# Kernel optimization log

Hardware: AMD Instinct MI355X
Metric: run time of the kernel (lower is better)

Reference implementation:

```python
import jax, jax.numpy as jnp
import numpy as np

N_EMBD = 512
N_HEAD = 8


def setup_inputs() -> dict:
    key = jax.random.key(0)
    k_x, k_aw, k_ab, k_pw, k_pb = jax.random.split(key, 5)
    B, T, E = 4, 2048, N_EMBD
    s = 1.0 / np.sqrt(E)
    return {
        "x": jax.random.normal(k_x, (B, T, E), dtype=jnp.float32),
        # torch Linear weight is [out, in]; store transposed for x @ W
        "c_attn_w": jax.random.uniform(k_aw, (E, 3 * E), jnp.float32, -s, s),
        "c_attn_b": jax.random.uniform(k_ab, (3 * E,), jnp.float32, -s, s),
        "c_proj_w": jax.random.uniform(k_pw, (E, E), jnp.float32, -s, s),
        "c_proj_b": jax.random.uniform(k_pb, (E,), jnp.float32, -s, s),
    }


def reference(x, c_attn_w, c_attn_b, c_proj_w, c_proj_b):
    B, T, E = x.shape
    H = N_HEAD
    D = E // H
    qkv = x @ c_attn_w + c_attn_b                      # [B,T,3E]
    q, k, v = jnp.split(qkv, 3, axis=2)
    # [B,T,E] -> [B,H,T,D]
    q = q.reshape(B, T, H, D).transpose(0, 2, 1, 3)
    k = k.reshape(B, T, H, D).transpose(0, 2, 1, 3)
    v = v.reshape(B, T, H, D).transpose(0, 2, 1, 3)
    scale = 1.0 / np.sqrt(D).astype(np.float32)
    scores = jnp.einsum("bhqd,bhkd->bhqk", q, k) * scale
    causal = jnp.tril(jnp.ones((T, T), dtype=bool))    # [T,T]
    scores = jnp.where(causal, scores, -jnp.inf)
    attn = jax.nn.softmax(scores, axis=-1)             # [B,H,T,T]
    y = jnp.einsum("bhqk,bhkd->bhqd", attn, v)         # [B,H,T,D]
    y = y.transpose(0, 2, 1, 3).reshape(B, T, E)
    return y @ c_proj_w + c_proj_b
```

## Files before the change

kernel.cpp:

```cpp
#include <hip/hip_runtime.h>
#include <math.h>

#define N_EMBD 512
#define N_HEAD 8
#define SEQ_T  2048
#define BATCH  4
#define QKV_LD 1536

typedef __attribute__((ext_vector_type(8))) short bf16x8;
typedef __attribute__((ext_vector_type(4))) float f32x4;

#define CL 0.18033688f

__device__ __forceinline__ unsigned short f2bf(float f) {
    union { float f; unsigned int u; } x; x.f = f;
    return (unsigned short)((x.u + 0x7FFFu + ((x.u >> 16) & 1u)) >> 16);
}
__device__ __forceinline__ unsigned pack_trunc(float a, float b) {
    union { float f; unsigned u; } x, y; x.f = a; y.f = b;
    return __builtin_amdgcn_perm(y.u, x.u, 0x07060302u);
}
__device__ __forceinline__ bf16x8 scale_frag(bf16x8 v, float c) {
    bf16x8 r;
    #pragma unroll
    for (int i = 0; i < 8; ++i) {
        union { unsigned u; float f; } x;
        x.u = ((unsigned)(unsigned short)v[i]) << 16;
        r[i] = (short)f2bf(x.f * c);
    }
    return r;
}

__device__ __forceinline__ void gl_lds16(const void* g, void* s) {
    __builtin_amdgcn_global_load_lds(
        (const __attribute__((address_space(1))) void*)g,
        (__attribute__((address_space(3))) void*)s, 16, 0, 0);
}

__global__ __launch_bounds__(256) void prep(
    const float* __restrict__ w1, unsigned short* __restrict__ w1t,
    const float* __restrict__ w2, unsigned short* __restrict__ w2t)
{
    __shared__ float t[32][33];
    const int bx = blockIdx.x, tid = threadIdx.x;
    const float* W; unsigned short* Wt; int N, tt, nb;
    if (bx < 768) { tt = bx;       W = w1; Wt = w1t; N = 1536; nb = 48; }
    else          { tt = bx - 768; W = w2; Wt = w2t; N = 512;  nb = 16; }
    const int n0 = (tt % nb) * 32, k0 = (tt / nb) * 32;
    const int tx = tid & 31, ty = tid >> 5;
    #pragma unroll
    for (int i = 0; i < 4; ++i)
        t[ty + i * 8][tx] = W[(size_t)(k0 + ty + i * 8) * N + n0 + tx];
    __syncthreads();
    #pragma unroll
    for (int i = 0; i < 4; ++i)
        Wt[(size_t)(n0 + ty + i * 8) * 512 + k0 + tx] = f2bf(t[tx][ty + i * 8]);
}

template <int BM, int BN, bool CVT_A, bool BF16_OUT>
__global__ __launch_bounds__(256) void gemm_mfma(
    const void* __restrict__ Asrc,
    const unsigned short* __restrict__ Bt,
    const float* __restrict__ bias,
    void* __restrict__ C, int N, int K,
    int xcdRows)
{
    constexpr int WMT = BM / 32, WNT = BN / 32;
    constexpr int SA = BM * 8 / 256, SB = BN * 8 / 256;
    __shared__ unsigned short As[BM * 64];
    __shared__ unsigned short Bs[BN * 64];

    const int tid  = threadIdx.x;
    const int wave = tid >> 6, lane = tid & 63;
    const int low  = lane & 15, quad = lane >> 4;
    const int wm   = (wave & 1) * (BM / 2), wn = (wave >> 1) * (BN / 2);

    const int xcd    = blockIdx.x & 7;
    const int within = blockIdx.x >> 3;
    const int rowBlk = xcd * xcdRows + (within % xcdRows);
    const int colBlk = within / xcdRows;
    const int row0 = rowBlk * BM, col0 = colBlk * BN;

    size_t a_src[SA]; int a_dst[SA];
    #pragma unroll
    for (int s = 0; s < SA; ++s) {
        const int p = tid + 256 * s;
        const int m = p >> 3, q = p & 7;
        a_src[s] = (size_t)(row0 + m) * K + q * 8;
        a_dst[s] = m * 64 + (q ^ (m & 7)) * 8;
    }
    size_t b_src[SB]; int b_dst[SB];
    #pragma unroll
    for (int s = 0; s < SB; ++s) {
        const int p = tid + 256 * s;
        const int m = p >> 3, q = p & 7;
        b_src[s] = (size_t)(col0 + m) * K + q * 8;
        b_dst[s] = m * 64 + (q ^ (m & 7)) * 8;
    }

    f32x4 acc[WMT][WNT];
    #pragma unroll
    for (int i = 0; i < WMT; ++i)
        #pragma unroll
        for (int j = 0; j < WNT; ++j) acc[i][j] = (f32x4){0.f, 0.f, 0.f, 0.f};

    bf16x8 ar[SA], br[SB];
    const float*          af32 = (const float*)Asrc;
    const unsigned short* a16  = (const unsigned short*)Asrc;

    #pragma unroll
    for (int s = 0; s < SA; ++s) {
        if (CVT_A) {
            const float4 f0 = *(const float4*)(af32 + a_src[s]);
            const float4 f1 = *(const float4*)(af32 + a_src[s] + 4);
            union { uint4 v; bf16x8 h; } u;
            u.v.x = pack_trunc(f0.x, f0.y); u.v.y = pack_trunc(f0.z, f0.w);
            u.v.z = pack_trunc(f1.x, f1.y); u.v.w = pack_trunc(f1.z, f1.w);
            ar[s] = u.h;
        } else {
            ar[s] = *(const bf16x8*)(a16 + a_src[s]);
        }
    }
    #pragma unroll
    for (int s = 0; s < SB; ++s) br[s] = *(const bf16x8*)(Bt + b_src[s]);

    const int NIT = K >> 6;
    for (int it = 0; it < NIT; ++it) {
        __syncthreads();
        #pragma unroll
        for (int s = 0; s < SA; ++s) *(bf16x8*)&As[a_dst[s]] = ar[s];
        #pragma unroll
        for (int s = 0; s < SB; ++s) *(bf16x8*)&Bs[b_dst[s]] = br[s];
        __syncthreads();

        if (it + 1 < NIT) {
            const int ko = (it + 1) * 64;
            #pragma unroll
            for (int s = 0; s < SA; ++s) {
                if (CVT_A) {
                    const float4 f0 = *(const float4*)(af32 + a_src[s] + ko);
                    const float4 f1 = *(const float4*)(af32 + a_src[s] + ko + 4);
                    union { uint4 v; bf16x8 h; } u;
                    u.v.x = pack_trunc(f0.x, f0.y); u.v.y = pack_trunc(f0.z, f0.w);
                    u.v.z = pack_trunc(f1.x, f1.y); u.v.w = pack_trunc(f1.z, f1.w);
                    ar[s] = u.h;
                } else {
                    ar[s] = *(const bf16x8*)(a16 + a_src[s] + ko);
                }
            }
            #pragma unroll
            for (int s = 0; s < SB; ++s) br[s] = *(const bf16x8*)(Bt + b_src[s] + ko);
        }

        #pragma unroll
        for (int h = 0; h < 2; ++h) {
            bf16x8 af[WMT], bfr[WNT];
            #pragma unroll
            for (int t = 0; t < WMT; ++t)
                af[t] = *(const bf16x8*)
                    &As[(wm + t * 16 + low) * 64 + (((h * 4 + quad) ^ (low & 7)) * 8)];
            #pragma unroll
            for (int t = 0; t < WNT; ++t)
                bfr[t] = *(const bf16x8*)
                    &Bs[(wn + t * 16 + low) * 64 + (((h * 4 + quad) ^ (low & 7)) * 8)];
            #pragma unroll
            for (int i = 0; i < WMT; ++i)
                #pragma unroll
                for (int j = 0; j < WNT; ++j)
                    acc[i][j] = __builtin_amdgcn_mfma_f32_16x16x32_bf16(
                        af[i], bfr[j], acc[i][j], 0, 0, 0);
        }
    }

    float bv[WNT];
    #pragma unroll
    for (int j = 0; j < WNT; ++j) bv[j] = bias[col0 + wn + j * 16 + low];
    #pragma unroll
    for (int i = 0; i < WMT; ++i)
        #pragma unroll
        for (int r = 0; r < 4; ++r) {
            const size_t row = row0 + wm + i * 16 + quad * 4 + r;
            #pragma unroll
            for (int j = 0; j < WNT; ++j) {
                const int col = col0 + wn + j * 16 + low;
                const float v = acc[i][j][r] + bv[j];
                if (BF16_OUT)
                    ((unsigned short*)C)[row * N + col] = f2bf(v);
                else
                    ((float*)C)[row * N + col] = v;
            }
        }
}

template <bool MASK>
__device__ __forceinline__ void tile_step(
    const bf16x8 kf[4][2], const bf16x8 qf0, const bf16x8 qf1,
    int thr, int quad, int low, unsigned short* ps)
{
    f32x4 s[4];
    #pragma unroll
    for (int st = 0; st < 4; ++st) {
        f32x4 a = (f32x4){0.f, 0.f, 0.f, 0.f};
        a = __builtin_amdgcn_mfma_f32_16x16x32_bf16(kf[st][0], qf0, a, 0, 0, 0);
        a = __builtin_amdgcn_mfma_f32_16x16x32_bf16(kf[st][1], qf1, a, 0, 0, 0);
        s[st] = a;
    }
    #pragma unroll
    for (int st = 0; st < 4; ++st) {
        float p[4];
        #pragma unroll
        for (int r = 0; r < 4; ++r) {
            float v = s[st][r];
            if (MASK) v = (st * 16 + r <= thr) ? v : -1e30f;
            p[r] = __builtin_amdgcn_exp2f(v);
        }
        uint2 pk;
        pk.x = pack_trunc(p[0], p[1]);
        pk.y = pack_trunc(p[2], p[3]);
        *(uint2*)&ps[low * 72 + st * 16 + quad * 4] = pk;
    }
}

__device__ __forceinline__ void pv_step(
    const bf16x8 vf[4][2], const unsigned short* ps, int quad, int low,
    f32x4* o, f32x4& lacc, const bf16x8 ones)
{
    const bf16x8 p0 = *(const bf16x8*)&ps[low * 72 + quad * 8];
    const bf16x8 p1 = *(const bf16x8*)&ps[low * 72 + quad * 8 + 32];
    #pragma unroll
    for (int t = 0; t < 4; ++t) {
        o[t] = __builtin_amdgcn_mfma_f32_16x16x32_bf16(p0, vf[t][0], o[t], 0, 0, 0);
        o[t] = __builtin_amdgcn_mfma_f32_16x16x32_bf16(p1, vf[t][1], o[t], 0, 0, 0);
    }
    lacc = __builtin_amdgcn_mfma_f32_16x16x32_bf16(p0, ones, lacc, 0, 0, 0);
    lacc = __builtin_amdgcn_mfma_f32_16x16x32_bf16(p1, ones, lacc, 0, 0, 0);
}

__global__ __launch_bounds__(256) void attn_mfma(
    const unsigned short* __restrict__ qkv,
    unsigned short* __restrict__ y)
{
    const int bh  = blockIdx.x & 31;
    const int pa  = blockIdx.x >> 5;
    const int b   = bh >> 3, h = bh & 7;
    const int qA0 = pa * 64;
    const int qB0 = (31 - pa) * 64;
    const int nA  = pa + 1, nB = 32 - pa;
    const int tid = threadIdx.x;
    const int wave = tid >> 6, lane = tid & 63;
    const int low  = lane & 15, quad = lane >> 4;

    __shared__ unsigned short Ks[2][64 * 64];
    __shared__ unsigned short Vt[2][64 * 64];
    __shared__ unsigned short PsA[4][16 * 72];
    __shared__ unsigned short PsB[4][16 * 72];

    const size_t base = (size_t)b * SEQ_T * QKV_LD + h * 64;
    const unsigned short* qp = qkv + base;
    const unsigned short* kp = qkv + base + 512;
    const unsigned short* vp = qkv + base + 1024;

    const int qmyA = qA0 + wave * 16 + low;
    const int qmyB = qB0 + wave * 16 + low;

    const bf16x8 qfA0 = scale_frag(*(const bf16x8*)(qp + (size_t)qmyA * QKV_LD + quad * 8), CL);
    const bf16x8 qfA1 = scale_frag(*(const bf16x8*)(qp + (size_t)qmyA * QKV_LD + quad * 8 + 32), CL);
    const bf16x8 qfB0 = scale_frag(*(const bf16x8*)(qp + (size_t)qmyB * QKV_LD + quad * 8), CL);
    const bf16x8 qfB1 = scale_frag(*(const bf16x8*)(qp + (size_t)qmyB * QKV_LD + quad * 8 + 32), CL);

    bf16x8 ones;
    #pragma unroll
    for (int i = 0; i < 8; ++i) ones[i] = (short)0x3F80;

    const int d0 = wave * 8;
    unsigned short* psA = &PsA[wave][0];
    unsigned short* psB = &PsB[wave][0];

    bf16x8 vr0 = *(const bf16x8*)(vp + (size_t)lane * QKV_LD + d0);
    bf16x8 vr1 = *(const bf16x8*)(vp + (size_t)lane * QKV_LD + d0 + 32);
    {
        #pragma unroll
        for (int ii = 0; ii < 2; ++ii) {
            const int row = wave * 16 + ii * 8 + (lane >> 3);
            const int o   = (lane & 7) ^ (lane >> 3);
            gl_lds16(kp + (size_t)row * QKV_LD + o * 8, &Ks[0][(wave * 2 + ii) * 512]);
        }
        #pragma unroll
        for (int ii = 0; ii < 8; ++ii) {
            const int po = ((lane >> 3) ^ ii) * 8 + (lane & 7);
            Vt[0][((d0 + ii) << 6) + po]      = (unsigned short)vr0[ii];
            Vt[0][((d0 + 32 + ii) << 6) + po] = (unsigned short)vr1[ii];
        }
        if (nB > 1) {
            vr0 = *(const bf16x8*)(vp + (size_t)(64 + lane) * QKV_LD + d0);
            vr1 = *(const bf16x8*)(vp + (size_t)(64 + lane) * QKV_LD + d0 + 32);
        }
    }
    __syncthreads();

    f32x4 oA[4], oB[4], lA, lB;
    #pragma unroll
    for (int t = 0; t < 4; ++t) {
        oA[t] = (f32x4){0.f, 0.f, 0.f, 0.f};
        oB[t] = (f32x4){0.f, 0.f, 0.f, 0.f};
    }
    lA = (f32x4){0.f, 0.f, 0.f, 0.f};
    lB = (f32x4){0.f, 0.f, 0.f, 0.f};

    for (int kc = 0; kc < nB; ++kc) {
        const int cur = kc & 1;
        unsigned short* ksc = &Ks[cur][0];
        unsigned short* vtc = &Vt[cur][0];

        if (kc + 1 < nB) {
            const int key1 = (kc + 1) * 64;
            #pragma unroll
            for (int ii = 0; ii < 2; ++ii) {
                const int row = wave * 16 + ii * 8 + (lane >> 3);
                const int o   = (lane & 7) ^ (lane >> 3);
                gl_lds16(kp + (size_t)(key1 + row) * QKV_LD + o * 8,
                         &Ks[cur ^ 1][(wave * 2 + ii) * 512]);
            }
            unsigned short* vtn = &Vt[cur ^ 1][0];
            #pragma unroll
            for (int ii = 0; ii < 8; ++ii) {
                const int po = ((lane >> 3) ^ ii) * 8 + (lane & 7);
                vtn[((d0 + ii) << 6) + po]      = (unsigned short)vr0[ii];
                vtn[((d0 + 32 + ii) << 6) + po] = (unsigned short)vr1[ii];
            }
        }
        if (kc + 2 < nB) {
            const int key2 = (kc + 2) * 64;
            vr0 = *(const bf16x8*)(vp + (size_t)(key2 + lane) * QKV_LD + d0);
            vr1 = *(const bf16x8*)(vp + (size_t)(key2 + lane) * QKV_LD + d0 + 32);
        }

        const int key0 = kc * 64;
        bf16x8 kf[4][2];
        #pragma unroll
        for (int t = 0; t < 4; ++t)
            #pragma unroll
            for (int i = 0; i < 2; ++i)
                kf[t][i] = *(const bf16x8*)
                    &ksc[((t * 16 + low) << 6) + (((quad + 4 * i) ^ (low & 7)) << 3)];

        if (kc < nA) {
            if (kc == nA - 1)
                tile_step<true >(kf, qfA0, qfA1, qmyA - key0 - quad * 4, quad, low, psA);
            else
                tile_step<false>(kf, qfA0, qfA1, 0, quad, low, psA);
        }
        if (kc == nB - 1)
            tile_step<true >(kf, qfB0, qfB1, qmyB - key0 - quad * 4, quad, low, psB);
        else
            tile_step<false>(kf, qfB0, qfB1, 0, quad, low, psB);

        asm volatile("" ::: "memory");

        bf16x8 vf[4][2];
        #pragma unroll
        for (int t = 0; t < 4; ++t)
            #pragma unroll
            for (int i = 0; i < 2; ++i)
                vf[t][i] = *(const bf16x8*)
                    &vtc[((t * 16 + low) << 6) + (((quad + 4 * i) ^ (low & 7)) << 3)];

        if (kc < nA) pv_step(vf, psA, quad, low, oA, lA, ones);
        pv_step(vf, psB, quad, low, oB, lB, ones);
        __syncthreads();
    }

    #pragma unroll
    for (int r = 0; r < 4; ++r) {
        const float rlA = 1.f / lA[r];
        const int qrow = qA0 + wave * 16 + quad * 4 + r;
        unsigned short* yp = y + (size_t)(b * SEQ_T + qrow) * N_EMBD + h * 64 + low;
        #pragma unroll
        for (int t = 0; t < 4; ++t) yp[16 * t] = f2bf(oA[t][r] * rlA);
    }
    #pragma unroll
    for (int r = 0; r < 4; ++r) {
        const float rlB = 1.f / lB[r];
        const int qrow = qB0 + wave * 16 + quad * 4 + r;
        unsigned short* yp = y + (size_t)(b * SEQ_T + qrow) * N_EMBD + h * 64 + low;
        #pragma unroll
        for (int t = 0; t < 4; ++t) yp[16 * t] = f2bf(oB[t][r] * rlB);
    }
}

extern "C" void kernel_launch(void* const* d_in, const int* in_sizes, int n_in,
                              void* d_out, int out_size, void* d_ws, size_t ws_size,
                              hipStream_t stream)
{
    const float* x      = (const float*)d_in[0];
    const float* attn_w = (const float*)d_in[1];
    const float* attn_b = (const float*)d_in[2];
    const float* proj_w = (const float*)d_in[3];
    const float* proj_b = (const float*)d_in[4];
    float*       out    = (float*)d_out;

    char* ws = (char*)d_ws;
    unsigned short* qkv_bf = (unsigned short*)(ws);
    unsigned short* y_bf   = (unsigned short*)(ws + 25165824);
    unsigned short* w1t    = (unsigned short*)(ws + 33554432);
    unsigned short* w2t    = (unsigned short*)(ws + 35127296);

    prep<<<1024, 256, 0, stream>>>(attn_w, w1t, proj_w, w2t);

    gemm_mfma<128, 128, true, true><<<dim3(768), 256, 0, stream>>>(
        x, w1t, attn_b, qkv_bf, QKV_LD, N_EMBD, 8);

    attn_mfma<<<dim3(512), 256, 0, stream>>>(qkv_bf, y_bf);

    gemm_mfma<64, 128, false, false><<<dim3(512), 256, 0, stream>>>(
        y_bf, w2t, proj_b, out, N_EMBD, N_EMBD, 16);
}
```

Baseline: 143.6 us.

## Write V transposed from QKV GEMM and run attention from registers without LDS

The QKV GEMM epilogue now stores Q and K in a 1024-wide buffer and writes V transposed into a separate [B, E, T] buffer. The attention kernel then loads K and V fragments straight from global memory into registers, prefetching one tile ahead, with no LDS staging and no per-tile block barrier. P stays in registers as the A operand of the PV MFMA, and the row sum comes from a scalar add of the truncated P instead of the ones-MFMA. Work is split so two waves take key halves and two take query halves, followed by a cross-wave reduction through LDS at the end. The costs are uncoalesced scattered stores for the V transpose, K/V global reads repeated across waves, and higher register pressure under launch bounds of 2.

After: 166.0 us. 15.6% more time.

```diff
diff --git a/kernel.cpp b/kernel.cpp
--- a/kernel.cpp
+++ b/kernel.cpp
@@ -5,7 +5,7 @@
 #define N_HEAD 8
 #define SEQ_T  2048
 #define BATCH  4
-#define QKV_LD 1536
+#define QK_LD  1024
 
 typedef __attribute__((ext_vector_type(8))) short bf16x8;
 typedef __attribute__((ext_vector_type(4))) float f32x4;
@@ -29,12 +29,6 @@
         r[i] = (short)f2bf(x.f * c);
     }
     return r;
-}
-
-__device__ __forceinline__ void gl_lds16(const void* g, void* s) {
-    __builtin_amdgcn_global_load_lds(
-        (const __attribute__((address_space(1))) void*)g,
-        (__attribute__((address_space(3))) void*)s, 16, 0, 0);
 }
 
 __global__ __launch_bounds__(256) void prep(
@@ -57,13 +51,13 @@
         Wt[(size_t)(n0 + ty + i * 8) * 512 + k0 + tx] = f2bf(t[tx][ty + i * 8]);
 }
 
-template <int BM, int BN, bool CVT_A, bool BF16_OUT>
+template <int BM, int BN, bool CVT_A, int OMODE>
 __global__ __launch_bounds__(256) void gemm_mfma(
     const void* __restrict__ Asrc,
     const unsigned short* __restrict__ Bt,
     const float* __restrict__ bias,
-    void* __restrict__ C, int N, int K,
-    int xcdRows)
+    void* __restrict__ C, unsigned short* __restrict__ Cv,
+    int N, int K, int xcdRows)
 {
     constexpr int WMT = BM / 32, WNT = BN / 32;
     constexpr int SA = BM * 8 / 256, SB = BN * 8 / 256;
@@ -175,69 +169,73 @@
     float bv[WNT];
     #pragma unroll
     for (int j = 0; j < WNT; ++j) bv[j] = bias[col0 + wn + j * 16 + low];
+    const bool isV = (OMODE == 2) && (col0 >= 1024);
     #pragma unroll
     for (int i = 0; i < WMT; ++i)
         #pragma unroll
         for (int r = 0; r < 4; ++r) {
-            const size_t row = row0 + wm + i * 16 + quad * 4 + r;
+            const int row = row0 + wm + i * 16 + quad * 4 + r;
             #pragma unroll
             for (int j = 0; j < WNT; ++j) {
                 const int col = col0 + wn + j * 16 + low;
                 const float v = acc[i][j][r] + bv[j];
-                if (BF16_OUT)
-                    ((unsigned short*)C)[row * N + col] = f2bf(v);
-                else
-                    ((float*)C)[row * N + col] = v;
+                if (OMODE == 0) {
+                    ((float*)C)[(size_t)row * N + col] = v;
+                } else if (OMODE == 1) {
+                    ((unsigned short*)C)[(size_t)row * N + col] = f2bf(v);
+                } else {
+                    if (isV)
+                        Cv[((size_t)((row >> 11) * 512 + col - 1024) << 11)
+                           + (row & 2047)] = f2bf(v);
+                    else
+                        ((unsigned short*)C)[(size_t)row * QK_LD + col] = f2bf(v);
+                }
             }
         }
 }
 
-template <bool MASK>
-__device__ __forceinline__ void tile_step(
-    const bf16x8 kf[4][2], const bf16x8 qf0, const bf16x8 qf1,
-    int thr, int quad, int low, unsigned short* ps)
+template<bool MASK>
+__device__ __forceinline__ void qk_step(
+    const bf16x8 k00, const bf16x8 k01, const bf16x8 k10, const bf16x8 k11,
+    const bf16x8 (&qf)[2][2], bf16x8 (&pf)[2], float (&lp)[2],
+    const int qrel0, const int koffb)
 {
-    f32x4 s[4];
-    #pragma unroll
-    for (int st = 0; st < 4; ++st) {
-        f32x4 a = (f32x4){0.f, 0.f, 0.f, 0.f};
-        a = __builtin_amdgcn_mfma_f32_16x16x32_bf16(kf[st][0], qf0, a, 0, 0, 0);
-        a = __builtin_amdgcn_mfma_f32_16x16x32_bf16(kf[st][1], qf1, a, 0, 0, 0);
-        s[st] = a;
-    }
-    #pragma unroll
-    for (int st = 0; st < 4; ++st) {
-        float p[4];
+    #pragma unroll
+    for (int qb = 0; qb < 2; ++qb) {
+        f32x4 s0 = (f32x4){0.f, 0.f, 0.f, 0.f};
+        f32x4 s1 = (f32x4){0.f, 0.f, 0.f, 0.f};
+        s0 = __builtin_amdgcn_mfma_f32_16x16x32_bf16(k00, qf[qb][0], s0, 0, 0, 0);
+        s0 = __builtin_amdgcn_mfma_f32_16x16x32_bf16(k01, qf[qb][1], s0, 0, 0, 0);
+        s1 = __builtin_amdgcn_mfma_f32_16x16x32_bf16(k10, qf[qb][0], s1, 0, 0, 0);
+        s1 = __builtin_amdgcn_mfma_f32_16x16x32_bf16(k11, qf[qb][1], s1, 0, 0, 0);
+        float p[8];
         #pragma unroll
         for (int r = 0; r < 4; ++r) {
-            float v = s[st][r];
-            if (MASK) v = (st * 16 + r <= thr) ? v : -1e30f;
-            p[r] = __builtin_amdgcn_exp2f(v);
-        }
-        uint2 pk;
-        pk.x = pack_trunc(p[0], p[1]);
-        pk.y = pack_trunc(p[2], p[3]);
-        *(uint2*)&ps[low * 72 + st * 16 + quad * 4] = pk;
-    }
-}
-
-__device__ __forceinline__ void pv_step(
-    const bf16x8 vf[4][2], const unsigned short* ps, int quad, int low,
-    f32x4* o, f32x4& lacc, const bf16x8 ones)
-{
-    const bf16x8 p0 = *(const bf16x8*)&ps[low * 72 + quad * 8];
-    const bf16x8 p1 = *(const bf16x8*)&ps[low * 72 + quad * 8 + 32];
-    #pragma unroll
-    for (int t = 0; t < 4; ++t) {
-        o[t] = __builtin_amdgcn_mfma_f32_16x16x32_bf16(p0, vf[t][0], o[t], 0, 0, 0);
-        o[t] = __builtin_amdgcn_mfma_f32_16x16x32_bf16(p1, vf[t][1], o[t], 0, 0, 0);
-    }
-    lacc = __builtin_amdgcn_mfma_f32_16x16x32_bf16(p0, ones, lacc, 0, 0, 0);
-    lacc = __builtin_amdgcn_mfma_f32_16x16x32_bf16(p1, ones, lacc, 0, 0, 0);
-}
-
-__global__ __launch_bounds__(256) void attn_mfma(
-    const unsigned short* __restrict__ qkv,
+            float v0 = s0[r], v1 = s1[r];
+            if (MASK) {
+                const int qrel = qrel0 + qb * 16;
+                if (koffb + r     > qrel) v0 = -1e30f;
+                if (koffb + r + 4 > qrel) v1 = -1e30f;
+            }
+            p[r]     = __builtin_amdgcn_exp2f(v0);
+            p[r + 4] = __builtin_amdgcn_exp2f(v1);
+        }
+        #pragma unroll
+        for (int e = 0; e < 8; ++e) {
+            union { float f; unsigned u; } c; c.f = p[e];
+            c.u &= 0xFFFF0000u; p[e] = c.f;
+        }
+        lp[qb] += ((p[0] + p[1]) + (p[2] + p[3])) + ((p[4] + p[5]) + (p[6] + p[7]));
+        union { uint4 v; bf16x8 h; } u;
+        u.v.x = pack_trunc(p[0], p[1]); u.v.y = pack_trunc(p[2], p[3]);
+        u.v.z = pack_trunc(p[4], p[5]); u.v.w = pack_trunc(p[6], p[7]);
+        pf[qb] = u.h;
+    }
+}
+
+__global__ __launch_bounds__(256, 2) void attn_mfma(
+    const unsigned short* __restrict__ qk,
+    const unsigned short* __restrict__ vT,
     unsigned short* __restrict__ y)
 {
     const int bh  = blockIdx.x & 31;
@@ -249,142 +247,149 @@
     const int tid = threadIdx.x;
     const int wave = tid >> 6, lane = tid & 63;
     const int low  = lane & 15, quad = lane >> 4;
-
-    __shared__ unsigned short Ks[2][64 * 64];
-    __shared__ unsigned short Vt[2][64 * 64];
-    __shared__ unsigned short PsA[4][16 * 72];
-    __shared__ unsigned short PsB[4][16 * 72];
-
-    const size_t base = (size_t)b * SEQ_T * QKV_LD + h * 64;
-    const unsigned short* qp = qkv + base;
-    const unsigned short* kp = qkv + base + 512;
-    const unsigned short* vp = qkv + base + 1024;
-
-    const int qmyA = qA0 + wave * 16 + low;
-    const int qmyB = qB0 + wave * 16 + low;
-
-    const bf16x8 qfA0 = scale_frag(*(const bf16x8*)(qp + (size_t)qmyA * QKV_LD + quad * 8), CL);
-    const bf16x8 qfA1 = scale_frag(*(const bf16x8*)(qp + (size_t)qmyA * QKV_LD + quad * 8 + 32), CL);
-    const bf16x8 qfB0 = scale_frag(*(const bf16x8*)(qp + (size_t)qmyB * QKV_LD + quad * 8), CL);
-    const bf16x8 qfB1 = scale_frag(*(const bf16x8*)(qp + (size_t)qmyB * QKV_LD + quad * 8 + 32), CL);
-
-    bf16x8 ones;
-    #pragma unroll
-    for (int i = 0; i < 8; ++i) ones[i] = (short)0x3F80;
-
-    const int d0 = wave * 8;
-    unsigned short* psA = &PsA[wave][0];
-    unsigned short* psB = &PsB[wave][0];
-
-    bf16x8 vr0 = *(const bf16x8*)(vp + (size_t)lane * QKV_LD + d0);
-    bf16x8 vr1 = *(const bf16x8*)(vp + (size_t)lane * QKV_LD + d0 + 32);
-    {
-        #pragma unroll
-        for (int ii = 0; ii < 2; ++ii) {
-            const int row = wave * 16 + ii * 8 + (lane >> 3);
-            const int o   = (lane & 7) ^ (lane >> 3);
-            gl_lds16(kp + (size_t)row * QKV_LD + o * 8, &Ks[0][(wave * 2 + ii) * 512]);
-        }
-        #pragma unroll
-        for (int ii = 0; ii < 8; ++ii) {
-            const int po = ((lane >> 3) ^ ii) * 8 + (lane & 7);
-            Vt[0][((d0 + ii) << 6) + po]      = (unsigned short)vr0[ii];
-            Vt[0][((d0 + 32 + ii) << 6) + po] = (unsigned short)vr1[ii];
-        }
-        if (nB > 1) {
-            vr0 = *(const bf16x8*)(vp + (size_t)(64 + lane) * QKV_LD + d0);
-            vr1 = *(const bf16x8*)(vp + (size_t)(64 + lane) * QKV_LD + d0 + 32);
-        }
+    const int kh   = wave & 1, qh = wave >> 1;
+
+    __shared__ float oBuf[2][64 * 66];
+    __shared__ float lBuf[2][2][64];
+
+    const size_t base = (size_t)b * SEQ_T * QK_LD + h * 64;
+    const unsigned short* qp = qk + base;
+    const unsigned short* kp = qk + base + 512;
+    const unsigned short* vp = vT + ((size_t)(b * 512 + h * 64) << 11);
+
+    bf16x8 qf[2][2][2];
+    #pragma unroll
+    for (int s = 0; s < 2; ++s) {
+        const int q0 = (s ? qB0 : qA0) + qh * 32;
+        #pragma unroll
+        for (int qb = 0; qb < 2; ++qb) {
+            const size_t qr = (size_t)(q0 + qb * 16 + low) * QK_LD;
+            #pragma unroll
+            for (int dh = 0; dh < 2; ++dh)
+                qf[s][qb][dh] = scale_frag(
+                    *(const bf16x8*)(qp + qr + dh * 32 + quad * 8), CL);
+        }
+    }
+
+    const int rowperm = ((low >> 2) << 3) + (low & 3);
+    const unsigned short* kbase =
+        kp + (size_t)(kh * 32 + rowperm) * QK_LD + quad * 8;
+    const int koffb = kh * 32 + quad * 8;
+    const unsigned short* vrow = vp + (size_t)low * SEQ_T + koffb;
+
+    bf16x8 kk[4], vv[4];
+    kk[0] = *(const bf16x8*)(kbase);
+    kk[1] = *(const bf16x8*)(kbase + 32);
+    kk[2] = *(const bf16x8*)(kbase + 4 * QK_LD);
+    kk[3] = *(const bf16x8*)(kbase + 4 * QK_LD + 32);
+    #pragma unroll
+    for (int t = 0; t < 4; ++t)
+        vv[t] = *(const bf16x8*)(vrow + (size_t)(t * 16) * SEQ_T);
+
+    f32x4 o[2][2][4];
+    #pragma unroll
+    for (int s = 0; s < 2; ++s)
+        #pragma unroll
+        for (int qb = 0; qb < 2; ++qb)
+            #pragma unroll
+            for (int t = 0; t < 4; ++t) o[s][qb][t] = (f32x4){0.f, 0.f, 0.f, 0.f};
+    float lp[2][2] = {{0.f, 0.f}, {0.f, 0.f}};
+
+    for (int kc = 0; kc < nB; ++kc) {
+        bf16x8 nk[4], nv[4];
+        const bool pfch = (kc + 1 < nB);
+        if (pfch) {
+            const unsigned short* kb = kbase + (size_t)(kc + 1) * (64 * QK_LD);
+            nk[0] = *(const bf16x8*)(kb);
+            nk[1] = *(const bf16x8*)(kb + 32);
+            nk[2] = *(const bf16x8*)(kb + 4 * QK_LD);
+            nk[3] = *(const bf16x8*)(kb + 4 * QK_LD + 32);
+            const unsigned short* vb = vrow + (kc + 1) * 64;
+            #pragma unroll
+            for (int t = 0; t < 4; ++t)
+                nv[t] = *(const bf16x8*)(vb + (size_t)(t * 16) * SEQ_T);
+        }
+
+        const int kc64 = kc * 64;
+        bf16x8 pA[2], pB[2];
+        const bool doA = (kc < nA);
+        if (doA) {
+            const int qrelA = qA0 + qh * 32 + low - kc64;
+            if (kc == nA - 1)
+                qk_step<true >(kk[0], kk[1], kk[2], kk[3], qf[0], pA, lp[0], qrelA, koffb);
+            else
+                qk_step<false>(kk[0], kk[1], kk[2], kk[3], qf[0], pA, lp[0], qrelA, koffb);
+        }
+        {
+            const int qrelB = qB0 + qh * 32 + low - kc64;
+            if (kc == nB - 1)
+                qk_step<true >(kk[0], kk[1], kk[2], kk[3], qf[1], pB, lp[1], qrelB, koffb);
+            else
+                qk_step<false>(kk[0], kk[1], kk[2], kk[3], qf[1], pB, lp[1], qrelB, koffb);
+        }
+
+        if (doA) {
+            #pragma unroll
+            for (int t = 0; t < 4; ++t) {
+                o[0][0][t] = __builtin_amdgcn_mfma_f32_16x16x32_bf16(pA[0], vv[t], o[0][0][t], 0, 0, 0);
+                o[0][1][t] = __builtin_amdgcn_mfma_f32_16x16x32_bf16(pA[1], vv[t], o[0][1][t], 0, 0, 0);
+            }
+        }
+        #pragma unroll
+        for (int t = 0; t < 4; ++t) {
+            o[1][0][t] = __builtin_amdgcn_mfma_f32_16x16x32_bf16(pB[0], vv[t], o[1][0][t], 0, 0, 0);
+            o[1][1][t] = __builtin_amdgcn_mfma_f32_16x16x32_bf16(pB[1], vv[t], o[1][1][t], 0, 0, 0);
+        }
+
+        if (pfch) {
+            #pragma unroll
+            for (int t = 0; t < 4; ++t) { kk[t] = nk[t]; vv[t] = nv[t]; }
+        }
+    }
+
+    #pragma unroll
+    for (int s = 0; s < 2; ++s)
+        #pragma unroll
+        for (int qb = 0; qb < 2; ++qb) {
+            float v = lp[s][qb];
+            v += __shfl_xor(v, 16);
+            v += __shfl_xor(v, 32);
+            if (quad == 0) lBuf[kh][qh][(s * 2 + qb) * 16 + low] = v;
+        }
+    if (kh == 1) {
+        #pragma unroll
+        for (int s = 0; s < 2; ++s)
+            #pragma unroll
+            for (int qb = 0; qb < 2; ++qb)
+                #pragma unroll
+                for (int t = 0; t < 4; ++t)
+                    #pragma unroll
+                    for (int r = 0; r < 4; ++r)
+                        oBuf[qh][((s * 2 + qb) * 16 + quad * 4 + r) * 66 + low + t * 16]
+                            = o[s][qb][t][r];
     }
     __syncthreads();
-
-    f32x4 oA[4], oB[4], lA, lB;
-    #pragma unroll
-    for (int t = 0; t < 4; ++t) {
-        oA[t] = (f32x4){0.f, 0.f, 0.f, 0.f};
-        oB[t] = (f32x4){0.f, 0.f, 0.f, 0.f};
-    }
-    lA = (f32x4){0.f, 0.f, 0.f, 0.f};
-    lB = (f32x4){0.f, 0.f, 0.f, 0.f};
-
-    for (int kc = 0; kc < nB; ++kc) {
-        const int cur = kc & 1;
-        unsigned short* ksc = &Ks[cur][0];
-        unsigned short* vtc = &Vt[cur][0];
-
-        if (kc + 1 < nB) {
-            const int key1 = (kc + 1) * 64;
-            #pragma unroll
-            for (int ii = 0; ii < 2; ++ii) {
-                const int row = wave * 16 + ii * 8 + (lane >> 3);
-                const int o   = (lane & 7) ^ (lane >> 3);
-                gl_lds16(kp + (size_t)(key1 + row) * QKV_LD + o * 8,
-                         &Ks[cur ^ 1][(wave * 2 + ii) * 512]);
+    if (kh == 0) {
+        #pragma unroll
+        for (int s = 0; s < 2; ++s) {
+            const int q0 = (s ? qB0 : qA0) + qh * 32;
+            #pragma unroll
+            for (int qb = 0; qb < 2; ++qb) {
+                #pragma unroll
+                for (int r = 0; r < 4; ++r) {
+                    const int ri = (s * 2 + qb) * 16 + quad * 4 + r;
+                    const float l = lBuf[0][qh][ri] + lBuf[1][qh][ri];
+                    const float rl = 1.f / l;
+                    const int qrow = q0 + qb * 16 + quad * 4 + r;
+                    unsigned short* yp =
+                        y + (size_t)(b * SEQ_T + qrow) * N_EMBD + h * 64 + low;
+                    #pragma unroll
+                    for (int t = 0; t < 4; ++t)
+                        yp[t * 16] = f2bf(
+                            (o[s][qb][t][r] + oBuf[qh][ri * 66 + low + t * 16]) * rl);
+                }
             }
-            unsigned short* vtn = &Vt[cur ^ 1][0];
-            #pragma unroll
-            for (int ii = 0; ii < 8; ++ii) {
-                const int po = ((lane >> 3) ^ ii) * 8 + (lane & 7);
-                vtn[((d0 + ii) << 6) + po]      = (unsigned short)vr0[ii];
-                vtn[((d0 + 32 + ii) << 6) + po] = (unsigned short)vr1[ii];
-            }
-        }
-        if (kc + 2 < nB) {
-            const int key2 = (kc + 2) * 64;
-            vr0 = *(const bf16x8*)(vp + (size_t)(key2 + lane) * QKV_LD + d0);
-            vr1 = *(const bf16x8*)(vp + (size_t)(key2 + lane) * QKV_LD + d0 + 32);
-        }
-
-        const int key0 = kc * 64;
-        bf16x8 kf[4][2];
-        #pragma unroll
-        for (int t = 0; t < 4; ++t)
-            #pragma unroll
-            for (int i = 0; i < 2; ++i)
-                kf[t][i] = *(const bf16x8*)
-                    &ksc[((t * 16 + low) << 6) + (((quad + 4 * i) ^ (low & 7)) << 3)];
-
-        if (kc < nA) {
-            if (kc == nA - 1)
-                tile_step<true >(kf, qfA0, qfA1, qmyA - key0 - quad * 4, quad, low, psA);
-            else
-                tile_step<false>(kf, qfA0, qfA1, 0, quad, low, psA);
-        }
-        if (kc == nB - 1)
-            tile_step<true >(kf, qfB0, qfB1, qmyB - key0 - quad * 4, quad, low, psB);
-        else
-            tile_step<false>(kf, qfB0, qfB1, 0, quad, low, psB);
-
-        asm volatile("" ::: "memory");
-
-        bf16x8 vf[4][2];
-        #pragma unroll
-        for (int t = 0; t < 4; ++t)
-            #pragma unroll
-            for (int i = 0; i < 2; ++i)
-                vf[t][i] = *(const bf16x8*)
-                    &vtc[((t * 16 + low) << 6) + (((quad + 4 * i) ^ (low & 7)) << 3)];
-
-        if (kc < nA) pv_step(vf, psA, quad, low, oA, lA, ones);
-        pv_step(vf, psB, quad, low, oB, lB, ones);
-        __syncthreads();
-    }
-
-    #pragma unroll
-    for (int r = 0; r < 4; ++r) {
-        const float rlA = 1.f / lA[r];
-        const int qrow = qA0 + wave * 16 + quad * 4 + r;
-        unsigned short* yp = y + (size_t)(b * SEQ_T + qrow) * N_EMBD + h * 64 + low;
-        #pragma unroll
-        for (int t = 0; t < 4; ++t) yp[16 * t] = f2bf(oA[t][r] * rlA);
-    }
-    #pragma unroll
-    for (int r = 0; r < 4; ++r) {
-        const float rlB = 1.f / lB[r];
-        const int qrow = qB0 + wave * 16 + quad * 4 + r;
-        unsigned short* yp = y + (size_t)(b * SEQ_T + qrow) * N_EMBD + h * 64 + low;
-        #pragma unroll
-        for (int t = 0; t < 4; ++t) yp[16 * t] = f2bf(oB[t][r] * rlB);
+        }
     }
 }
 
@@ -400,18 +405,19 @@
     float*       out    = (float*)d_out;
 
     char* ws = (char*)d_ws;
-    unsigned short* qkv_bf = (unsigned short*)(ws);
-    unsigned short* y_bf   = (unsigned short*)(ws + 25165824);
-    unsigned short* w1t    = (unsigned short*)(ws + 33554432);
-    unsigned short* w2t    = (unsigned short*)(ws + 35127296);
+    unsigned short* qk_bf = (unsigned short*)(ws);
+    unsigned short* vT    = (unsigned short*)(ws + 16777216);
+    unsigned short* y_bf  = (unsigned short*)(ws + 25165824);
+    unsigned short* w1t   = (unsigned short*)(ws + 33554432);
+    unsigned short* w2t   = (unsigned short*)(ws + 35127296);
 
     prep<<<1024, 256, 0, stream>>>(attn_w, w1t, proj_w, w2t);
 
-    gemm_mfma<128, 128, true, true><<<dim3(768), 256, 0, stream>>>(
-        x, w1t, attn_b, qkv_bf, QKV_LD, N_EMBD, 8);
-
-    attn_mfma<<<dim3(512), 256, 0, stream>>>(qkv_bf, y_bf);
-
-    gemm_mfma<64, 128, false, false><<<dim3(512), 256, 0, stream>>>(
-        y_bf, w2t, proj_b, out, N_EMBD, N_EMBD, 16);
-}
+    gemm_mfma<128, 128, true, 2><<<dim3(768), 256, 0, stream>>>(
+        x, w1t, attn_b, qk_bf, vT, 1536, N_EMBD, 8);
+
+    attn_mfma<<<dim3(512), 256, 0, stream>>>(qk_bf, vT, y_bf);
+
+    gemm_mfma<64, 128, false, 0><<<dim3(512), 256, 0, stream>>>(
+        y_bf, w2t, proj_b, out, nullptr, N_EMBD, N_EMBD, 16);
+}
```
